# Kernel tuning notes

Measured on AMD Instinct MI355X. Metric: run time of the kernel, lower is better.

## Reference

```python
import jax, jax.numpy as jnp
import numpy as np

D_MODEL = 1024
NUM_HEADS = 16
D_K = D_MODEL // NUM_HEADS


def setup_inputs() -> dict:
    key = jax.random.key(0)
    ks = jax.random.split(key, 9)
    B, S = 2, 2048
    s = 1.0 / np.sqrt(D_MODEL)
    inp = {
        "x": jax.random.normal(ks[0], (B, S, D_MODEL), dtype=jnp.float32),
        "Wq": jax.random.normal(ks[1], (D_MODEL, D_MODEL), dtype=jnp.float32) * s,
        "bq": jnp.zeros((D_MODEL,), dtype=jnp.float32),
        "Wk": jax.random.normal(ks[2], (D_MODEL, D_MODEL), dtype=jnp.float32) * s,
        "bk": jnp.zeros((D_MODEL,), dtype=jnp.float32),
        "Wv": jax.random.normal(ks[3], (D_MODEL, D_MODEL), dtype=jnp.float32) * s,
        "bv": jnp.zeros((D_MODEL,), dtype=jnp.float32),
        "Wo": jax.random.normal(ks[4], (D_MODEL, D_MODEL), dtype=jnp.float32) * s,
        "bo": jnpp if False else jnp.zeros((D_MODEL,), dtype=jnp.float32),
    }
    return inp


def reference(x, Wq, bq, Wk, bk, Wv, bv, Wo, bo):
    B, S, _ = x.shape
    H, Dk = NUM_HEADS, D_K

    def proj(W, b):
        # [B,S,D] -> [B,H,S,Dk]
        return (x @ W + b).reshape(B, S, H, Dk).transpose(0, 2, 1, 3)

    Q = proj(Wq, bq)
    K = proj(Wk, bk)
    V = proj(Wv, bv)

    scores = jnp.einsum("bhqd,bhkd->bhqk", Q, K) / np.sqrt(Dk)
    attn = jax.nn.softmax(scores, axis=-1)  # no mask, dropout p=0 (eval)
    out = jnp.einsum("bhqk,bhkd->bhqd", attn, V)
    out = out.transpose(0, 2, 1, 3).reshape(B, S, D_MODEL)
    return out @ Wo + bo
```

## Files before the change

kernel.cpp:

```cpp
#include <hip/hip_runtime.h>
#include <hip/hip_bf16.h>
#include <cstdint>
#include <math.h>

#define D_MODEL 1024
#define NHEADS  16
#define DK      64
#define BATCH   2
#define SEQ     2048
#define M_TOTAL (BATCH*SEQ)
#define NSPLIT  4
#define NTS     (SEQ/64/NSPLIT)

using f32x4  = __attribute__((ext_vector_type(4)))  float;
using f32x16 = __attribute__((ext_vector_type(16))) float;
using s16x8  = __attribute__((ext_vector_type(8)))  short;

#define CSC (0.125f * 1.44269504088896341f)

__device__ __forceinline__ unsigned short bf16r(float f) {
    __hip_bfloat16 h = __float2bfloat16(f);
    return *(unsigned short*)&h;
}
__device__ __forceinline__ uint32_t cvtpk(float lo, float hi) {
    uint32_t r;
    asm("v_cvt_pk_bf16_f32 %0, %1, %2" : "=v"(r) : "v"(lo), "v"(hi));
    return r;
}
__device__ __forceinline__ float b2f(unsigned short u) {
    uint32_t x = (uint32_t)u << 16;
    float f;
    __builtin_memcpy(&f, &x, 4);
    return f;
}

__global__ __launch_bounds__(256) void conv_x(const float* __restrict__ x,
                                              unsigned short* __restrict__ xb)
{
    const size_t i = ((size_t)blockIdx.x * 256 + threadIdx.x) * 8;
    const float4 a = *(const float4*)(x + i);
    const float4 b = *(const float4*)(x + i + 4);
    ushort4 r0, r1;
    r0.x = bf16r(a.x); r0.y = bf16r(a.y); r0.z = bf16r(a.z); r0.w = bf16r(a.w);
    r1.x = bf16r(b.x); r1.y = bf16r(b.y); r1.z = bf16r(b.z); r1.w = bf16r(b.w);
    *(ushort4*)(xb + i)     = r0;
    *(ushort4*)(xb + i + 4) = r1;
}

__global__ __launch_bounds__(256) void conv_wt(const float* __restrict__ W0, const float* __restrict__ W1,
                                               const float* __restrict__ W2, const float* __restrict__ W3,
                                               unsigned short* __restrict__ T0, unsigned short* __restrict__ T1,
                                               unsigned short* __restrict__ T2, unsigned short* __restrict__ T3)
{
    const float* W; unsigned short* T;
    switch (blockIdx.z) {
        case 0: W = W0; T = T0; break;
        case 1: W = W1; T = T1; break;
        case 2: W = W2; T = T2; break;
        default: W = W3; T = T3; break;
    }
    __shared__ float tile[32][33];
    const int t  = threadIdx.x;
    const int r  = t >> 3;
    const int c4 = (t & 7) * 4;
    const int k0 = blockIdx.x * 32;
    const int n0 = blockIdx.y * 32;

    const float4 v = *(const float4*)(W + (size_t)(k0 + r) * 1024 + n0 + c4);
    tile[r][c4 + 0] = v.x; tile[r][c4 + 1] = v.y; tile[r][c4 + 2] = v.z; tile[r][c4 + 3] = v.w;
    __syncthreads();
    ushort4 o;
    o.x = bf16r(tile[c4 + 0][r]);
    o.y = bf16r(tile[c4 + 1][r]);
    o.z = bf16r(tile[c4 + 2][r]);
    o.w = bf16r(tile[c4 + 3][r]);
    *(ushort4*)(T + (size_t)(n0 + r) * 1024 + k0 + c4) = o;
}

template<int OUT_BF16>
__device__ __forceinline__ void gemm_mfma_body(const unsigned short* __restrict__ A,
                                               const unsigned short* __restrict__ Bt,
                                               const float* __restrict__ bias,
                                               void* __restrict__ C,
                                               float oscale)
{
    __shared__ unsigned short As[128 * 64];
    __shared__ unsigned short Bs[128 * 64];

    const int t    = threadIdx.x;
    const int w    = t >> 6;
    const int lane = t & 63;
    const int ln   = lane & 15;
    const int g    = lane >> 4;
    const int wr   = w >> 1, wc = w & 1;
    const int m0   = blockIdx.y * 128;
    const int n0   = blockIdx.x * 128;

    f32x4 acc[4][4];
#pragma unroll
    for (int mi = 0; mi < 4; ++mi)
#pragma unroll
        for (int ni = 0; ni < 4; ++ni)
#pragma unroll
            for (int j = 0; j < 4; ++j) acc[mi][ni][j] = 0.f;

    const int lrow = lane >> 3;
    const int lchk = (lane & 7) ^ lrow;
    const unsigned short* Ag = A  + (size_t)(m0 + w * 32 + lrow) * 1024 + lchk * 8;
    const unsigned short* Bg = Bt + (size_t)(n0 + w * 32 + lrow) * 1024 + lchk * 8;

    for (int kt = 0; kt < 16; ++kt) {
        const int k0 = kt * 64;
#pragma unroll
        for (int i = 0; i < 4; ++i) {
            __builtin_amdgcn_global_load_lds(Ag + (size_t)i * 8 * 1024 + k0,
                                             &As[(w * 32 + i * 8) * 64], 16, 0, 0);
            __builtin_amdgcn_global_load_lds(Bg + (size_t)i * 8 * 1024 + k0,
                                             &Bs[(w * 32 + i * 8) * 64], 16, 0, 0);
        }
        __syncthreads();

#pragma unroll
        for (int ks = 0; ks < 2; ++ks) {
            s16x8 af[4], bf[4];
#pragma unroll
            for (int mi = 0; mi < 4; ++mi) {
                const int row = wr * 64 + mi * 16 + ln;
                af[mi] = *(const s16x8*)((const char*)As + row * 128 +
                                         (((ks * 4 + g) ^ (ln & 7)) * 16));
            }
#pragma unroll
            for (int ni = 0; ni < 4; ++ni) {
                const int row = wc * 64 + ni * 16 + ln;
                bf[ni] = *(const s16x8*)((const char*)Bs + row * 128 +
                                         (((ks * 4 + g) ^ (ln & 7)) * 16));
            }
#pragma unroll
            for (int mi = 0; mi < 4; ++mi)
#pragma unroll
                for (int ni = 0; ni < 4; ++ni)
                    acc[mi][ni] = __builtin_amdgcn_mfma_f32_16x16x32_bf16(
                        af[mi], bf[ni], acc[mi][ni], 0, 0, 0);
        }
        __syncthreads();
    }

#pragma unroll
    for (int ni = 0; ni < 4; ++ni) {
        const int n = n0 + wc * 64 + ni * 16 + ln;
        const float bn = bias[n];
#pragma unroll
        for (int mi = 0; mi < 4; ++mi) {
            const int m = m0 + wr * 64 + mi * 16 + g * 4;
#pragma unroll
            for (int j = 0; j < 4; ++j) {
                const float v = (acc[mi][ni][j] + bn) * oscale;
                if constexpr (OUT_BF16)
                    ((unsigned short*)C)[(size_t)(m + j) * 1024 + n] = bf16r(v);
                else
                    ((float*)C)[(size_t)(m + j) * 1024 + n] = v;
            }
        }
    }
}

__global__ __launch_bounds__(256) void qkv_mfma(const unsigned short* __restrict__ xb,
                                                const unsigned short* __restrict__ Wqt, const float* __restrict__ bq,
                                                const unsigned short* __restrict__ Wkt, const float* __restrict__ bk,
                                                const unsigned short* __restrict__ Wvt, const float* __restrict__ bv,
                                                unsigned short* __restrict__ Q,
                                                unsigned short* __restrict__ K,
                                                unsigned short* __restrict__ V)
{
    if (blockIdx.z == 0)      gemm_mfma_body<1>(xb, Wqt, bq, Q, CSC);
    else if (blockIdx.z == 1) gemm_mfma_body<1>(xb, Wkt, bk, K, 1.0f);
    else                      gemm_mfma_body<1>(xb, Wvt, bv, V, 1.0f);
}

__global__ __launch_bounds__(256) void oproj_mfma(const unsigned short* __restrict__ Ab,
                                                  const unsigned short* __restrict__ Wot,
                                                  const float* __restrict__ bo,
                                                  float* __restrict__ C)
{
    gemm_mfma_body<0>(Ab, Wot, bo, C, 1.0f);
}

__global__ __launch_bounds__(256, 4) void attn_mfma(const unsigned short* __restrict__ Qb,
                                                    const unsigned short* __restrict__ Kb,
                                                    const unsigned short* __restrict__ Vb,
                                                    unsigned short* __restrict__ O0,
                                                    unsigned short* __restrict__ O1,
                                                    unsigned short* __restrict__ O2,
                                                    unsigned short* __restrict__ O3,
                                                    float* __restrict__ lbuf)
{
    __shared__ unsigned short Klds [64 * 64];
    __shared__ unsigned short Vtlds[64 * 64];

    const int t   = threadIdx.x;
    const int wid = t >> 6;
    const int l   = t & 63;
    const int q32 = l & 31;
    const int hi  = l >> 5;

    const int bh = blockIdx.y;
    const int b  = bh >> 4;
    const int h  = bh & 15;
    const int sp = blockIdx.z;
    const int qbase = blockIdx.x * 128 + wid * 32;
    const size_t qrow = (size_t)(b * SEQ + qbase + q32);
    const size_t kv0  = (size_t)(b * SEQ) + (size_t)sp * (SEQ / NSPLIT);

    s16x8 qf[4];
    {
        const unsigned short* qp = Qb + qrow * D_MODEL + h * DK + 8 * hi;
#pragma unroll
        for (int ks = 0; ks < 4; ++ks) qf[ks] = *(const s16x8*)(qp + 16 * ks);
    }

    f32x16 ot0, ot1;
#pragma unroll
    for (int i = 0; i < 16; ++i) { ot0[i] = 0.f; ot1[i] = 0.f; }
    float lsum = 0.f;

    const int skey = t >> 3;
    const int sc8  = t & 7;
    const int vk2  = 2 * (t & 31);
    const int pk2  = (vk2 & ~12) | ((vk2 & 4) << 1) | ((vk2 & 8) >> 1);
    const int vd0  = 8 * (t >> 5);
    const unsigned short* Kg = Kb + (kv0 + skey) * D_MODEL + h * DK + 8 * sc8;
    const unsigned short* Vg = Vb + (kv0 + vk2) * D_MODEL + h * DK + vd0;
    char* const kw0 = (char*)Klds + skey * 128        + 16 * (sc8 ^ (skey & 7));
    char* const kw1 = (char*)Klds + (skey + 32) * 128 + 16 * (sc8 ^ (skey & 7));

    s16x8 kr0, kr1, vr0, vr1;

    auto load_regs = [&](int kt) {
        const size_t off = (size_t)kt * 64 * D_MODEL;
        kr0 = *(const s16x8*)(Kg + off);
        kr1 = *(const s16x8*)(Kg + off + (size_t)32 * D_MODEL);
        vr0 = *(const s16x8*)(Vg + off);
        vr1 = *(const s16x8*)(Vg + off + D_MODEL);
    };
    auto write_stage = [&]() {
        *(s16x8*)kw0 = kr0;
        *(s16x8*)kw1 = kr1;
#pragma unroll
        for (int i = 0; i < 8; ++i) {
            const int d = vd0 + i;
            const uint32_t val = (uint32_t)(unsigned short)vr0[i] |
                                 ((uint32_t)(unsigned short)vr1[i] << 16);
            *(uint32_t*)((char*)Vtlds + d * 128 +
                         16 * ((pk2 >> 3) ^ (d & 7)) + (pk2 & 7) * 2) = val;
        }
    };

    load_regs(0);
    write_stage();
    __syncthreads();

    for (int kt = 0; kt < NTS; ++kt) {
        if (kt < NTS - 1) load_regs(kt + 1);

        f32x16 s0, s1;
#pragma unroll
        for (int i = 0; i < 16; ++i) { s0[i] = 0.f; s1[i] = 0.f; }
        __builtin_amdgcn_s_setprio(1);
#pragma unroll
        for (int ks = 0; ks < 4; ++ks) {
            const int c = hi + 2 * ks;
            const s16x8 a0 = *(const s16x8*)((char*)Klds + q32 * 128 + 16 * (c ^ (q32 & 7)));
            const s16x8 a1 = *(const s16x8*)((char*)Klds + (q32 + 32) * 128 + 16 * (c ^ (q32 & 7)));
            s0 = __builtin_amdgcn_mfma_f32_32x32x16_bf16(a0, qf[ks], s0, 0, 0, 0);
            s1 = __builtin_amdgcn_mfma_f32_32x32x16_bf16(a1, qf[ks], s1, 0, 0, 0);
        }
        __builtin_amdgcn_s_setprio(0);

        float la = 0.f, lb = 0.f, lc = 0.f, ld = 0.f;
#pragma unroll
        for (int i = 0; i < 4; ++i) {
            s0[4 * i + 0] = exp2f(s0[4 * i + 0]); la += s0[4 * i + 0];
            s0[4 * i + 1] = exp2f(s0[4 * i + 1]); lb += s0[4 * i + 1];
            s0[4 * i + 2] = exp2f(s0[4 * i + 2]); lc += s0[4 * i + 2];
            s0[4 * i + 3] = exp2f(s0[4 * i + 3]); ld += s0[4 * i + 3];
            s1[4 * i + 0] = exp2f(s1[4 * i + 0]); la += s1[4 * i + 0];
            s1[4 * i + 1] = exp2f(s1[4 * i + 1]); lb += s1[4 * i + 1];
            s1[4 * i + 2] = exp2f(s1[4 * i + 2]); lc += s1[4 * i + 2];
            s1[4 * i + 3] = exp2f(s1[4 * i + 3]); ld += s1[4 * i + 3];
        }
        lsum += (la + lb) + (lc + ld);

        s16x8 pf[4];
        {
            union { uint32_t u[4]; s16x8 v; } F;
#pragma unroll
            for (int e = 0; e < 4; ++e) F.u[e] = cvtpk(s0[2 * e], s0[2 * e + 1]);
            pf[0] = F.v;
#pragma unroll
            for (int e = 0; e < 4; ++e) F.u[e] = cvtpk(s0[8 + 2 * e], s0[9 + 2 * e]);
            pf[1] = F.v;
#pragma unroll
            for (int e = 0; e < 4; ++e) F.u[e] = cvtpk(s1[2 * e], s1[2 * e + 1]);
            pf[2] = F.v;
#pragma unroll
            for (int e = 0; e < 4; ++e) F.u[e] = cvtpk(s1[8 + 2 * e], s1[9 + 2 * e]);
            pf[3] = F.v;
        }

        __builtin_amdgcn_s_setprio(1);
#pragma unroll
        for (int ks = 0; ks < 4; ++ks) {
            const int c = hi + 2 * ks;
            const s16x8 av0 = *(const s16x8*)((char*)Vtlds + q32 * 128 + 16 * (c ^ (q32 & 7)));
            const s16x8 av1 = *(const s16x8*)((char*)Vtlds + (q32 + 32) * 128 + 16 * (c ^ (q32 & 7)));
            ot0 = __builtin_amdgcn_mfma_f32_32x32x16_bf16(av0, pf[ks], ot0, 0, 0, 0);
            ot1 = __builtin_amdgcn_mfma_f32_32x32x16_bf16(av1, pf[ks], ot1, 0, 0, 0);
        }
        __builtin_amdgcn_s_setprio(0);

        __syncthreads();
        if (kt < NTS - 1) write_stage();
        __syncthreads();
    }

    const float ltot = lsum + __shfl_xor(lsum, 32);
    const size_t prow = (size_t)bh * SEQ + qbase + q32;
    if (hi == 0)
        lbuf[(size_t)sp * (BATCH * NHEADS * SEQ) + prow] = ltot;

    unsigned short* opb = (sp == 0) ? O0 : (sp == 1) ? O1 : (sp == 2) ? O2 : O3;
    unsigned short* op  = opb + prow * DK;
#pragma unroll
    for (int j = 0; j < 4; ++j) {
        uint2 st0, st1;
        st0.x = cvtpk(ot0[4 * j + 0], ot0[4 * j + 1]);
        st0.y = cvtpk(ot0[4 * j + 2], ot0[4 * j + 3]);
        st1.x = cvtpk(ot1[4 * j + 0], ot1[4 * j + 1]);
        st1.y = cvtpk(ot1[4 * j + 2], ot1[4 * j + 3]);
        *(uint2*)(op + 8 * j + 4 * hi)      = st0;
        *(uint2*)(op + 32 + 8 * j + 4 * hi) = st1;
    }
}

__global__ __launch_bounds__(256) void attn_combine(const unsigned short* __restrict__ O0,
                                                    const unsigned short* __restrict__ O1,
                                                    const unsigned short* __restrict__ O2,
                                                    const unsigned short* __restrict__ O3,
                                                    const float* __restrict__ lbuf,
                                                    unsigned short* __restrict__ Ab)
{
    const int tid = blockIdx.x * 256 + threadIdx.x;
    const int row = tid >> 3;
    const int d0  = (tid & 7) * 8;
    const size_t NROW = (size_t)BATCH * NHEADS * SEQ;

    const float rinv = 1.0f / (lbuf[row] + lbuf[NROW + row] +
                               lbuf[2 * NROW + row] + lbuf[3 * NROW + row]);

    const size_t src = (size_t)row * DK + d0;
    const ushort4 a0 = *(const ushort4*)(O0 + src);
    const ushort4 a1 = *(const ushort4*)(O0 + src + 4);
    const ushort4 b0 = *(const ushort4*)(O1 + src);
    const ushort4 b1 = *(const ushort4*)(O1 + src + 4);
    const ushort4 c0 = *(const ushort4*)(O2 + src);
    const ushort4 c1 = *(const ushort4*)(O2 + src + 4);
    const ushort4 e0 = *(const ushort4*)(O3 + src);
    const ushort4 e1 = *(const ushort4*)(O3 + src + 4);

    const int bh = row >> 11, s = row & 2047;
    const int b = bh >> 4, h = bh & 15;
    unsigned short* dst = Ab + ((size_t)(b * SEQ + s)) * D_MODEL + h * DK + d0;

    ushort4 o0, o1;
    o0.x = bf16r((b2f(a0.x) + b2f(b0.x) + b2f(c0.x) + b2f(e0.x)) * rinv);
    o0.y = bf16r((b2f(a0.y) + b2f(b0.y) + b2f(c0.y) + b2f(e0.y)) * rinv);
    o0.z = bf16r((b2f(a0.z) + b2f(b0.z) + b2f(c0.z) + b2f(e0.z)) * rinv);
    o0.w = bf16r((b2f(a0.w) + b2f(b0.w) + b2f(c0.w) + b2f(e0.w)) * rinv);
    o1.x = bf16r((b2f(a1.x) + b2f(b1.x) + b2f(c1.x) + b2f(e1.x)) * rinv);
    o1.y = bf16r((b2f(a1.y) + b2f(b1.y) + b2f(c1.y) + b2f(e1.y)) * rinv);
    o1.z = bf16r((b2f(a1.z) + b2f(b1.z) + b2f(c1.z) + b2f(e1.z)) * rinv);
    o1.w = bf16r((b2f(a1.w) + b2f(b1.w) + b2f(c1.w) + b2f(e1.w)) * rinv);
    *(ushort4*)(dst)     = o0;
    *(ushort4*)(dst + 4) = o1;
}

extern "C" void kernel_launch(void* const* d_in, const int* in_sizes, int n_in,
                              void* d_out, int out_size, void* d_ws, size_t ws_size,
                              hipStream_t stream)
{
    const float* x  = (const float*)d_in[0];
    const float* Wq = (const float*)d_in[1];
    const float* bq = (const float*)d_in[2];
    const float* Wk = (const float*)d_in[3];
    const float* bk = (const float*)d_in[4];
    const float* Wv = (const float*)d_in[5];
    const float* bv = (const float*)d_in[6];
    const float* Wo = (const float*)d_in[7];
    const float* bo = (const float*)d_in[8];

    float* out = (float*)d_out;

    const size_t mat  = (size_t)M_TOTAL * D_MODEL;
    const size_t wmat = (size_t)D_MODEL * D_MODEL;
    unsigned short* xb  = (unsigned short*)d_ws;
    unsigned short* Wqt = xb  + mat;
    unsigned short* Wkt = Wqt + wmat;
    unsigned short* Wvt = Wkt + wmat;
    unsigned short* Wot = Wvt + wmat;
    unsigned short* Qb  = Wot + wmat;
    unsigned short* Kb  = Qb  + mat;
    unsigned short* Vb  = Kb  + mat;
    unsigned short* Ab  = Vb  + mat;
    unsigned short* Op0 = Ab  + mat;
    unsigned short* Op1 = Op0 + mat;
    unsigned short* Op2 = xb;
    unsigned short* Op3 = (unsigned short*)d_out;
    float*          lbuf = (float*)Wqt;

    conv_x<<<dim3(2048), 256, 0, stream>>>(x, xb);
    conv_wt<<<dim3(32, 32, 4), 256, 0, stream>>>(Wq, Wk, Wv, Wo, Wqt, Wkt, Wvt, Wot);

    qkv_mfma<<<dim3(8, 32, 3), 256, 0, stream>>>(xb, Wqt, bq, Wkt, bk, Wvt, bv, Qb, Kb, Vb);

    attn_mfma<<<dim3(SEQ / 128, BATCH * NHEADS, NSPLIT), 256, 0, stream>>>(
        Qb, Kb, Vb, Op0, Op1, Op2, Op3, lbuf);

    attn_combine<<<dim3((BATCH * NHEADS * SEQ * 8) / 256), 256, 0, stream>>>(
        Op0, Op1, Op2, Op3, lbuf, Ab);

    oproj_mfma<<<dim3(8, 32), 256, 0, stream>>>(Ab, Wot, bo, out);
}
```

Before: 147.4 us.

## Halve attention KV split, double-buffer K via direct global-to-LDS loads, merge conversion kernels

```diff
diff --git a/kernel.cpp b/kernel.cpp
--- a/kernel.cpp
+++ b/kernel.cpp
@@ -9,7 +9,7 @@
 #define BATCH   2
 #define SEQ     2048
 #define M_TOTAL (BATCH*SEQ)
-#define NSPLIT  4
+#define NSPLIT  2
 #define NTS     (SEQ/64/NSPLIT)
 
 using f32x4  = __attribute__((ext_vector_type(4)))  float;
@@ -34,37 +34,45 @@
     return f;
 }
 
-__global__ __launch_bounds__(256) void conv_x(const float* __restrict__ x,
-                                              unsigned short* __restrict__ xb)
-{
-    const size_t i = ((size_t)blockIdx.x * 256 + threadIdx.x) * 8;
-    const float4 a = *(const float4*)(x + i);
-    const float4 b = *(const float4*)(x + i + 4);
-    ushort4 r0, r1;
-    r0.x = bf16r(a.x); r0.y = bf16r(a.y); r0.z = bf16r(a.z); r0.w = bf16r(a.w);
-    r1.x = bf16r(b.x); r1.y = bf16r(b.y); r1.z = bf16r(b.z); r1.w = bf16r(b.w);
-    *(ushort4*)(xb + i)     = r0;
-    *(ushort4*)(xb + i + 4) = r1;
-}
-
-__global__ __launch_bounds__(256) void conv_wt(const float* __restrict__ W0, const float* __restrict__ W1,
-                                               const float* __restrict__ W2, const float* __restrict__ W3,
-                                               unsigned short* __restrict__ T0, unsigned short* __restrict__ T1,
-                                               unsigned short* __restrict__ T2, unsigned short* __restrict__ T3)
-{
+__global__ __launch_bounds__(256) void conv_all(const float* __restrict__ x,
+                                                unsigned short* __restrict__ xb,
+                                                const float* __restrict__ W0, const float* __restrict__ W1,
+                                                const float* __restrict__ W2, const float* __restrict__ W3,
+                                                unsigned short* __restrict__ T0, unsigned short* __restrict__ T1,
+                                                unsigned short* __restrict__ T2, unsigned short* __restrict__ T3)
+{
+    __shared__ float tile[32][33];
+    const int bid = blockIdx.x;
+    const int t   = threadIdx.x;
+
+    if (bid < 2048) {
+        const size_t i = ((size_t)bid * 256 + t) * 8;
+        const float4 a = *(const float4*)(x + i);
+        const float4 b = *(const float4*)(x + i + 4);
+        ushort4 r0, r1;
+        r0.x = bf16r(a.x); r0.y = bf16r(a.y); r0.z = bf16r(a.z); r0.w = bf16r(a.w);
+        r1.x = bf16r(b.x); r1.y = bf16r(b.y); r1.z = bf16r(b.z); r1.w = bf16r(b.w);
+        *(ushort4*)(xb + i)     = r0;
+        *(ushort4*)(xb + i + 4) = r1;
+        return;
+    }
+
+    const int b2   = bid - 2048;
+    const int z    = b2 >> 10;
+    const int rest = b2 & 1023;
+    const int kblk = rest & 31;
+    const int nblk = rest >> 5;
     const float* W; unsigned short* T;
-    switch (blockIdx.z) {
+    switch (z) {
         case 0: W = W0; T = T0; break;
         case 1: W = W1; T = T1; break;
         case 2: W = W2; T = T2; break;
         default: W = W3; T = T3; break;
     }
-    __shared__ float tile[32][33];
-    const int t  = threadIdx.x;
     const int r  = t >> 3;
     const int c4 = (t & 7) * 4;
-    const int k0 = blockIdx.x * 32;
-    const int n0 = blockIdx.y * 32;
+    const int k0 = kblk * 32;
+    const int n0 = nblk * 32;
 
     const float4 v = *(const float4*)(W + (size_t)(k0 + r) * 1024 + n0 + c4);
     tile[r][c4 + 0] = v.x; tile[r][c4 + 1] = v.y; tile[r][c4 + 2] = v.z; tile[r][c4 + 3] = v.w;
@@ -190,11 +198,9 @@
                                                     const unsigned short* __restrict__ Vb,
                                                     unsigned short* __restrict__ O0,
                                                     unsigned short* __restrict__ O1,
-                                                    unsigned short* __restrict__ O2,
-                                                    unsigned short* __restrict__ O3,
                                                     float* __restrict__ lbuf)
 {
-    __shared__ unsigned short Klds [64 * 64];
+    __shared__ unsigned short Klds[2][64 * 64];
     __shared__ unsigned short Vtlds[64 * 64];
 
     const int t   = threadIdx.x;
@@ -223,28 +229,29 @@
     for (int i = 0; i < 16; ++i) { ot0[i] = 0.f; ot1[i] = 0.f; }
     float lsum = 0.f;
 
-    const int skey = t >> 3;
-    const int sc8  = t & 7;
+    const unsigned short* Kgl = Kb + (kv0 + wid * 16 + (l >> 3)) * D_MODEL
+                                   + h * DK + 8 * ((l & 7) ^ (l >> 3));
+    auto stage_K = [&](int kt, int buf) {
+        const size_t off = (size_t)kt * 64 * D_MODEL;
+#pragma unroll
+        for (int j = 0; j < 2; ++j)
+            __builtin_amdgcn_global_load_lds(Kgl + off + (size_t)j * 8 * D_MODEL,
+                                             &Klds[buf][(wid * 16 + j * 8) * 64],
+                                             16, 0, 0);
+    };
+
     const int vk2  = 2 * (t & 31);
     const int pk2  = (vk2 & ~12) | ((vk2 & 4) << 1) | ((vk2 & 8) >> 1);
     const int vd0  = 8 * (t >> 5);
-    const unsigned short* Kg = Kb + (kv0 + skey) * D_MODEL + h * DK + 8 * sc8;
     const unsigned short* Vg = Vb + (kv0 + vk2) * D_MODEL + h * DK + vd0;
-    char* const kw0 = (char*)Klds + skey * 128        + 16 * (sc8 ^ (skey & 7));
-    char* const kw1 = (char*)Klds + (skey + 32) * 128 + 16 * (sc8 ^ (skey & 7));
-
-    s16x8 kr0, kr1, vr0, vr1;
-
-    auto load_regs = [&](int kt) {
+
+    s16x8 vr0, vr1;
+    auto load_V = [&](int kt) {
         const size_t off = (size_t)kt * 64 * D_MODEL;
-        kr0 = *(const s16x8*)(Kg + off);
-        kr1 = *(const s16x8*)(Kg + off + (size_t)32 * D_MODEL);
         vr0 = *(const s16x8*)(Vg + off);
         vr1 = *(const s16x8*)(Vg + off + D_MODEL);
     };
-    auto write_stage = [&]() {
-        *(s16x8*)kw0 = kr0;
-        *(s16x8*)kw1 = kr1;
+    auto write_V = [&]() {
 #pragma unroll
         for (int i = 0; i < 8; ++i) {
             const int d = vd0 + i;
@@ -255,12 +262,16 @@
         }
     };
 
-    load_regs(0);
-    write_stage();
+    stage_K(0, 0);
+    load_V(0);
+    write_V();
     __syncthreads();
 
     for (int kt = 0; kt < NTS; ++kt) {
-        if (kt < NTS - 1) load_regs(kt + 1);
+        const int cur = kt & 1;
+        if (kt < NTS - 1) { stage_K(kt + 1, cur ^ 1); load_V(kt + 1); }
+
+        const char* Kl = (const char*)&Klds[cur][0];
 
         f32x16 s0, s1;
 #pragma unroll
@@ -269,8 +280,8 @@
 #pragma unroll
         for (int ks = 0; ks < 4; ++ks) {
             const int c = hi + 2 * ks;
-            const s16x8 a0 = *(const s16x8*)((char*)Klds + q32 * 128 + 16 * (c ^ (q32 & 7)));
-            const s16x8 a1 = *(const s16x8*)((char*)Klds + (q32 + 32) * 128 + 16 * (c ^ (q32 & 7)));
+            const s16x8 a0 = *(const s16x8*)(Kl + q32 * 128 + 16 * (c ^ (q32 & 7)));
+            const s16x8 a1 = *(const s16x8*)(Kl + (q32 + 32) * 128 + 16 * (c ^ (q32 & 7)));
             s0 = __builtin_amdgcn_mfma_f32_32x32x16_bf16(a0, qf[ks], s0, 0, 0, 0);
             s1 = __builtin_amdgcn_mfma_f32_32x32x16_bf16(a1, qf[ks], s1, 0, 0, 0);
         }
@@ -319,7 +330,7 @@
         __builtin_amdgcn_s_setprio(0);
 
         __syncthreads();
-        if (kt < NTS - 1) write_stage();
+        if (kt < NTS - 1) write_V();
         __syncthreads();
     }
 
@@ -328,8 +339,7 @@
     if (hi == 0)
         lbuf[(size_t)sp * (BATCH * NHEADS * SEQ) + prow] = ltot;
 
-    unsigned short* opb = (sp == 0) ? O0 : (sp == 1) ? O1 : (sp == 2) ? O2 : O3;
-    unsigned short* op  = opb + prow * DK;
+    unsigned short* op = ((sp == 0) ? O0 : O1) + prow * DK;
 #pragma unroll
     for (int j = 0; j < 4; ++j) {
         uint2 st0, st1;
@@ -344,8 +354,6 @@
 
 __global__ __launch_bounds__(256) void attn_combine(const unsigned short* __restrict__ O0,
                                                     const unsigned short* __restrict__ O1,
-                                                    const unsigned short* __restrict__ O2,
-                                                    const unsigned short* __restrict__ O3,
                                                     const float* __restrict__ lbuf,
                                                     unsigned short* __restrict__ Ab)
 {
@@ -354,32 +362,27 @@
     const int d0  = (tid & 7) * 8;
     const size_t NROW = (size_t)BATCH * NHEADS * SEQ;
 
-    const float rinv = 1.0f / (lbuf[row] + lbuf[NROW + row] +
-                               lbuf[2 * NROW + row] + lbuf[3 * NROW + row]);
+    const float rinv = 1.0f / (lbuf[row] + lbuf[NROW + row]);
 
     const size_t src = (size_t)row * DK + d0;
     const ushort4 a0 = *(const ushort4*)(O0 + src);
     const ushort4 a1 = *(const ushort4*)(O0 + src + 4);
     const ushort4 b0 = *(const ushort4*)(O1 + src);
     const ushort4 b1 = *(const ushort4*)(O1 + src + 4);
-    const ushort4 c0 = *(const ushort4*)(O2 + src);
-    const ushort4 c1 = *(const ushort4*)(O2 + src + 4);
-    const ushort4 e0 = *(const ushort4*)(O3 + src);
-    const ushort4 e1 = *(const ushort4*)(O3 + src + 4);
 
     const int bh = row >> 11, s = row & 2047;
     const int b = bh >> 4, h = bh & 15;
     unsigned short* dst = Ab + ((size_t)(b * SEQ + s)) * D_MODEL + h * DK + d0;
 
     ushort4 o0, o1;
-    o0.x = bf16r((b2f(a0.x) + b2f(b0.x) + b2f(c0.x) + b2f(e0.x)) * rinv);
-    o0.y = bf16r((b2f(a0.y) + b2f(b0.y) + b2f(c0.y) + b2f(e0.y)) * rinv);
-    o0.z = bf16r((b2f(a0.z) + b2f(b0.z) + b2f(c0.z) + b2f(e0.z)) * rinv);
-    o0.w = bf16r((b2f(a0.w) + b2f(b0.w) + b2f(c0.w) + b2f(e0.w)) * rinv);
-    o1.x = bf16r((b2f(a1.x) + b2f(b1.x) + b2f(c1.x) + b2f(e1.x)) * rinv);
-    o1.y = bf16r((b2f(a1.y) + b2f(b1.y) + b2f(c1.y) + b2f(e1.y)) * rinv);
-    o1.z = bf16r((b2f(a1.z) + b2f(b1.z) + b2f(c1.z) + b2f(e1.z)) * rinv);
-    o1.w = bf16r((b2f(a1.w) + b2f(b1.w) + b2f(c1.w) + b2f(e1.w)) * rinv);
+    o0.x = bf16r((b2f(a0.x) + b2f(b0.x)) * rinv);
+    o0.y = bf16r((b2f(a0.y) + b2f(b0.y)) * rinv);
+    o0.z = bf16r((b2f(a0.z) + b2f(b0.z)) * rinv);
+    o0.w = bf16r((b2f(a0.w) + b2f(b0.w)) * rinv);
+    o1.x = bf16r((b2f(a1.x) + b2f(b1.x)) * rinv);
+    o1.y = bf16r((b2f(a1.y) + b2f(b1.y)) * rinv);
+    o1.z = bf16r((b2f(a1.z) + b2f(b1.z)) * rinv);
+    o1.w = bf16r((b2f(a1.w) + b2f(b1.w)) * rinv);
     *(ushort4*)(dst)     = o0;
     *(ushort4*)(dst + 4) = o1;
 }
@@ -413,20 +416,17 @@
     unsigned short* Ab  = Vb  + mat;
     unsigned short* Op0 = Ab  + mat;
     unsigned short* Op1 = Op0 + mat;
-    unsigned short* Op2 = xb;
-    unsigned short* Op3 = (unsigned short*)d_out;
-    float*          lbuf = (float*)Wqt;
-
-    conv_x<<<dim3(2048), 256, 0, stream>>>(x, xb);
-    conv_wt<<<dim3(32, 32, 4), 256, 0, stream>>>(Wq, Wk, Wv, Wo, Wqt, Wkt, Wvt, Wot);
+    float*          lbuf = (float*)xb;
+
+    conv_all<<<dim3(6144), 256, 0, stream>>>(x, xb, Wq, Wk, Wv, Wo, Wqt, Wkt, Wvt, Wot);
 
     qkv_mfma<<<dim3(8, 32, 3), 256, 0, stream>>>(xb, Wqt, bq, Wkt, bk, Wvt, bv, Qb, Kb, Vb);
 
     attn_mfma<<<dim3(SEQ / 128, BATCH * NHEADS, NSPLIT), 256, 0, stream>>>(
-        Qb, Kb, Vb, Op0, Op1, Op2, Op3, lbuf);
+        Qb, Kb, Vb, Op0, Op1, lbuf);
 
     attn_combine<<<dim3((BATCH * NHEADS * SEQ * 8) / 256), 256, 0, stream>>>(
-        Op0, Op1, Op2, Op3, lbuf, Ab);
+        Op0, Op1, lbuf, Ab);
 
     oproj_mfma<<<dim3(8, 32), 256, 0, stream>>>(Ab, Wot, bo, out);
 }
```

Measured after the change: 140.6 us. -4.6%, faster.

## Write K/V in MFMA fragment layout and load directly from global in attention

Applied to the files above, without the earlier changes.

```diff
diff --git a/kernel.cpp b/kernel.cpp
--- a/kernel.cpp
+++ b/kernel.cpp
@@ -34,37 +34,45 @@
     return f;
 }
 
-__global__ __launch_bounds__(256) void conv_x(const float* __restrict__ x,
-                                              unsigned short* __restrict__ xb)
-{
-    const size_t i = ((size_t)blockIdx.x * 256 + threadIdx.x) * 8;
-    const float4 a = *(const float4*)(x + i);
-    const float4 b = *(const float4*)(x + i + 4);
-    ushort4 r0, r1;
-    r0.x = bf16r(a.x); r0.y = bf16r(a.y); r0.z = bf16r(a.z); r0.w = bf16r(a.w);
-    r1.x = bf16r(b.x); r1.y = bf16r(b.y); r1.z = bf16r(b.z); r1.w = bf16r(b.w);
-    *(ushort4*)(xb + i)     = r0;
-    *(ushort4*)(xb + i + 4) = r1;
-}
-
-__global__ __launch_bounds__(256) void conv_wt(const float* __restrict__ W0, const float* __restrict__ W1,
-                                               const float* __restrict__ W2, const float* __restrict__ W3,
-                                               unsigned short* __restrict__ T0, unsigned short* __restrict__ T1,
-                                               unsigned short* __restrict__ T2, unsigned short* __restrict__ T3)
-{
+__global__ __launch_bounds__(256) void conv_all(const float* __restrict__ x,
+                                                unsigned short* __restrict__ xb,
+                                                const float* __restrict__ W0, const float* __restrict__ W1,
+                                                const float* __restrict__ W2, const float* __restrict__ W3,
+                                                unsigned short* __restrict__ T0, unsigned short* __restrict__ T1,
+                                                unsigned short* __restrict__ T2, unsigned short* __restrict__ T3)
+{
+    __shared__ float tile[32][33];
+    const int bid = blockIdx.x;
+    const int t   = threadIdx.x;
+
+    if (bid < 2048) {
+        const size_t i = ((size_t)bid * 256 + t) * 8;
+        const float4 a = *(const float4*)(x + i);
+        const float4 b = *(const float4*)(x + i + 4);
+        ushort4 r0, r1;
+        r0.x = bf16r(a.x); r0.y = bf16r(a.y); r0.z = bf16r(a.z); r0.w = bf16r(a.w);
+        r1.x = bf16r(b.x); r1.y = bf16r(b.y); r1.z = bf16r(b.z); r1.w = bf16r(b.w);
+        *(ushort4*)(xb + i)     = r0;
+        *(ushort4*)(xb + i + 4) = r1;
+        return;
+    }
+
+    const int b2   = bid - 2048;
+    const int z    = b2 >> 10;
+    const int rest = b2 & 1023;
+    const int kblk = rest & 31;
+    const int nblk = rest >> 5;
     const float* W; unsigned short* T;
-    switch (blockIdx.z) {
+    switch (z) {
         case 0: W = W0; T = T0; break;
         case 1: W = W1; T = T1; break;
         case 2: W = W2; T = T2; break;
         default: W = W3; T = T3; break;
     }
-    __shared__ float tile[32][33];
-    const int t  = threadIdx.x;
     const int r  = t >> 3;
     const int c4 = (t & 7) * 4;
-    const int k0 = blockIdx.x * 32;
-    const int n0 = blockIdx.y * 32;
+    const int k0 = kblk * 32;
+    const int n0 = nblk * 32;
 
     const float4 v = *(const float4*)(W + (size_t)(k0 + r) * 1024 + n0 + c4);
     tile[r][c4 + 0] = v.x; tile[r][c4 + 1] = v.y; tile[r][c4 + 2] = v.z; tile[r][c4 + 3] = v.w;
@@ -77,7 +85,7 @@
     *(ushort4*)(T + (size_t)(n0 + r) * 1024 + k0 + c4) = o;
 }
 
-template<int OUT_BF16>
+template<int MODE>
 __device__ __forceinline__ void gemm_mfma_body(const unsigned short* __restrict__ A,
                                                const unsigned short* __restrict__ Bt,
                                                const float* __restrict__ bias,
@@ -155,10 +163,24 @@
 #pragma unroll
             for (int j = 0; j < 4; ++j) {
                 const float v = (acc[mi][ni][j] + bn) * oscale;
-                if constexpr (OUT_BF16)
-                    ((unsigned short*)C)[(size_t)(m + j) * 1024 + n] = bf16r(v);
-                else
-                    ((float*)C)[(size_t)(m + j) * 1024 + n] = v;
+                const int mj = m + j;
+                if constexpr (MODE == 0) {
+                    ((float*)C)[(size_t)mj * 1024 + n] = v;
+                } else if constexpr (MODE == 1) {
+                    ((unsigned short*)C)[(size_t)mj * 1024 + n] = bf16r(v);
+                } else if constexpr (MODE == 2) {
+                    const int bh = ((mj >> 11) << 4) | (n >> 6);
+                    const size_t off = (size_t)(bh * 32 + ((mj >> 6) & 31)) * 4096
+                                     + ((n >> 3) & 7) * 512 + (mj & 63) * 8 + (n & 7);
+                    ((unsigned short*)C)[off] = bf16r(v);
+                } else {
+                    const int bh = ((mj >> 11) << 4) | (n >> 6);
+                    const int k6 = mj & 63;
+                    const int x  = (k6 & ~12) | ((k6 & 4) << 1) | ((k6 & 8) >> 1);
+                    const size_t off = (size_t)(bh * 32 + ((mj >> 6) & 31)) * 4096
+                                     + (x >> 3) * 512 + (n & 63) * 8 + (x & 7);
+                    ((unsigned short*)C)[off] = bf16r(v);
+                }
             }
         }
     }
@@ -169,12 +191,12 @@
                                                 const unsigned short* __restrict__ Wkt, const float* __restrict__ bk,
                                                 const unsigned short* __restrict__ Wvt, const float* __restrict__ bv,
                                                 unsigned short* __restrict__ Q,
-                                                unsigned short* __restrict__ K,
-                                                unsigned short* __restrict__ V)
-{
-    if (blockIdx.z == 0)      gemm_mfma_body<1>(xb, Wqt, bq, Q, CSC);
-    else if (blockIdx.z == 1) gemm_mfma_body<1>(xb, Wkt, bk, K, 1.0f);
-    else                      gemm_mfma_body<1>(xb, Wvt, bv, V, 1.0f);
+                                                unsigned short* __restrict__ Kt,
+                                                unsigned short* __restrict__ Vt)
+{
+    if (blockIdx.z == 0)      gemm_mfma_body<1>(xb, Wqt, bq, Q,  CSC);
+    else if (blockIdx.z == 1) gemm_mfma_body<2>(xb, Wkt, bk, Kt, 1.0f);
+    else                      gemm_mfma_body<3>(xb, Wvt, bv, Vt, 1.0f);
 }
 
 __global__ __launch_bounds__(256) void oproj_mfma(const unsigned short* __restrict__ Ab,
@@ -186,17 +208,14 @@
 }
 
 __global__ __launch_bounds__(256, 4) void attn_mfma(const unsigned short* __restrict__ Qb,
-                                                    const unsigned short* __restrict__ Kb,
-                                                    const unsigned short* __restrict__ Vb,
+                                                    const unsigned short* __restrict__ Kt,
+                                                    const unsigned short* __restrict__ Vt,
                                                     unsigned short* __restrict__ O0,
                                                     unsigned short* __restrict__ O1,
                                                     unsigned short* __restrict__ O2,
                                                     unsigned short* __restrict__ O3,
                                                     float* __restrict__ lbuf)
 {
-    __shared__ unsigned short Klds [64 * 64];
-    __shared__ unsigned short Vtlds[64 * 64];
-
     const int t   = threadIdx.x;
     const int wid = t >> 6;
     const int l   = t & 63;
@@ -209,7 +228,6 @@
     const int sp = blockIdx.z;
     const int qbase = blockIdx.x * 128 + wid * 32;
     const size_t qrow = (size_t)(b * SEQ + qbase + q32);
-    const size_t kv0  = (size_t)(b * SEQ) + (size_t)sp * (SEQ / NSPLIT);
 
     s16x8 qf[4];
     {
@@ -223,44 +241,18 @@
     for (int i = 0; i < 16; ++i) { ot0[i] = 0.f; ot1[i] = 0.f; }
     float lsum = 0.f;
 
-    const int skey = t >> 3;
-    const int sc8  = t & 7;
-    const int vk2  = 2 * (t & 31);
-    const int pk2  = (vk2 & ~12) | ((vk2 & 4) << 1) | ((vk2 & 8) >> 1);
-    const int vd0  = 8 * (t >> 5);
-    const unsigned short* Kg = Kb + (kv0 + skey) * D_MODEL + h * DK + 8 * sc8;
-    const unsigned short* Vg = Vb + (kv0 + vk2) * D_MODEL + h * DK + vd0;
-    char* const kw0 = (char*)Klds + skey * 128        + 16 * (sc8 ^ (skey & 7));
-    char* const kw1 = (char*)Klds + (skey + 32) * 128 + 16 * (sc8 ^ (skey & 7));
-
-    s16x8 kr0, kr1, vr0, vr1;
-
-    auto load_regs = [&](int kt) {
-        const size_t off = (size_t)kt * 64 * D_MODEL;
-        kr0 = *(const s16x8*)(Kg + off);
-        kr1 = *(const s16x8*)(Kg + off + (size_t)32 * D_MODEL);
-        vr0 = *(const s16x8*)(Vg + off);
-        vr1 = *(const s16x8*)(Vg + off + D_MODEL);
-    };
-    auto write_stage = [&]() {
-        *(s16x8*)kw0 = kr0;
-        *(s16x8*)kw1 = kr1;
-#pragma unroll
-        for (int i = 0; i < 8; ++i) {
-            const int d = vd0 + i;
-            const uint32_t val = (uint32_t)(unsigned short)vr0[i] |
-                                 ((uint32_t)(unsigned short)vr1[i] << 16);
-            *(uint32_t*)((char*)Vtlds + d * 128 +
-                         16 * ((pk2 >> 3) ^ (d & 7)) + (pk2 & 7) * 2) = val;
-        }
-    };
-
-    load_regs(0);
-    write_stage();
-    __syncthreads();
+    const unsigned short* kp = Kt + ((size_t)bh * 32 + sp * NTS) * 4096
+                                  + hi * 512 + q32 * 8;
+    const unsigned short* vp = Vt + ((size_t)bh * 32 + sp * NTS) * 4096
+                                  + hi * 512 + q32 * 8;
 
     for (int kt = 0; kt < NTS; ++kt) {
-        if (kt < NTS - 1) load_regs(kt + 1);
+        s16x8 ka0[4], ka1[4];
+#pragma unroll
+        for (int ks = 0; ks < 4; ++ks) {
+            ka0[ks] = *(const s16x8*)(kp + 2 * ks * 512);
+            ka1[ks] = *(const s16x8*)(kp + 2 * ks * 512 + 256);
+        }
 
         f32x16 s0, s1;
 #pragma unroll
@@ -268,13 +260,17 @@
         __builtin_amdgcn_s_setprio(1);
 #pragma unroll
         for (int ks = 0; ks < 4; ++ks) {
-            const int c = hi + 2 * ks;
-            const s16x8 a0 = *(const s16x8*)((char*)Klds + q32 * 128 + 16 * (c ^ (q32 & 7)));
-            const s16x8 a1 = *(const s16x8*)((char*)Klds + (q32 + 32) * 128 + 16 * (c ^ (q32 & 7)));
-            s0 = __builtin_amdgcn_mfma_f32_32x32x16_bf16(a0, qf[ks], s0, 0, 0, 0);
-            s1 = __builtin_amdgcn_mfma_f32_32x32x16_bf16(a1, qf[ks], s1, 0, 0, 0);
+            s0 = __builtin_amdgcn_mfma_f32_32x32x16_bf16(ka0[ks], qf[ks], s0, 0, 0, 0);
+            s1 = __builtin_amdgcn_mfma_f32_32x32x16_bf16(ka1[ks], qf[ks], s1, 0, 0, 0);
         }
         __builtin_amdgcn_s_setprio(0);
+
+        s16x8 va0[4], va1[4];
+#pragma unroll
+        for (int ks = 0; ks < 4; ++ks) {
+            va0[ks] = *(const s16x8*)(vp + 2 * ks * 512);
+            va1[ks] = *(const s16x8*)(vp + 2 * ks * 512 + 256);
+        }
 
         float la = 0.f, lb = 0.f, lc = 0.f, ld = 0.f;
 #pragma unroll
@@ -310,17 +306,13 @@
         __builtin_amdgcn_s_setprio(1);
 #pragma unroll
         for (int ks = 0; ks < 4; ++ks) {
-            const int c = hi + 2 * ks;
-            const s16x8 av0 = *(const s16x8*)((char*)Vtlds + q32 * 128 + 16 * (c ^ (q32 & 7)));
-            const s16x8 av1 = *(const s16x8*)((char*)Vtlds + (q32 + 32) * 128 + 16 * (c ^ (q32 & 7)));
-            ot0 = __builtin_amdgcn_mfma_f32_32x32x16_bf16(av0, pf[ks], ot0, 0, 0, 0);
-            ot1 = __builtin_amdgcn_mfma_f32_32x32x16_bf16(av1, pf[ks], ot1, 0, 0, 0);
+            ot0 = __builtin_amdgcn_mfma_f32_32x32x16_bf16(va0[ks], pf[ks], ot0, 0, 0, 0);
+            ot1 = __builtin_amdgcn_mfma_f32_32x32x16_bf16(va1[ks], pf[ks], ot1, 0, 0, 0);
         }
         __builtin_amdgcn_s_setprio(0);
 
-        __syncthreads();
-        if (kt < NTS - 1) write_stage();
-        __syncthreads();
+        kp += 4096;
+        vp += 4096;
     }
 
     const float ltot = lsum + __shfl_xor(lsum, 32);
@@ -408,22 +400,21 @@
     unsigned short* Wvt = Wkt + wmat;
     unsigned short* Wot = Wvt + wmat;
     unsigned short* Qb  = Wot + wmat;
-    unsigned short* Kb  = Qb  + mat;
-    unsigned short* Vb  = Kb  + mat;
-    unsigned short* Ab  = Vb  + mat;
+    unsigned short* Kt  = Qb  + mat;
+    unsigned short* Vt  = Kt  + mat;
+    unsigned short* Ab  = Vt  + mat;
     unsigned short* Op0 = Ab  + mat;
     unsigned short* Op1 = Op0 + mat;
     unsigned short* Op2 = xb;
     unsigned short* Op3 = (unsigned short*)d_out;
     float*          lbuf = (float*)Wqt;
 
-    conv_x<<<dim3(2048), 256, 0, stream>>>(x, xb);
-    conv_wt<<<dim3(32, 32, 4), 256, 0, stream>>>(Wq, Wk, Wv, Wo, Wqt, Wkt, Wvt, Wot);
-
-    qkv_mfma<<<dim3(8, 32, 3), 256, 0, stream>>>(xb, Wqt, bq, Wkt, bk, Wvt, bv, Qb, Kb, Vb);
+    conv_all<<<dim3(6144), 256, 0, stream>>>(x, xb, Wq, Wk, Wv, Wo, Wqt, Wkt, Wvt, Wot);
+
+    qkv_mfma<<<dim3(8, 32, 3), 256, 0, stream>>>(xb, Wqt, bq, Wkt, bk, Wvt, bv, Qb, Kt, Vt);
 
     attn_mfma<<<dim3(SEQ / 128, BATCH * NHEADS, NSPLIT), 256, 0, stream>>>(
-        Qb, Kb, Vb, Op0, Op1, Op2, Op3, lbuf);
+        Qb, Kt, Vt, Op0, Op1, Op2, Op3, lbuf);
 
     attn_combine<<<dim3((BATCH * NHEADS * SEQ * 8) / 256), 256, 0, stream>>>(
         Op0, Op1, Op2, Op3, lbuf, Ab);
```

After: 172.1 us. 1.17x slower.
